# Kernel tuning notes

Measured on AMD Instinct MI355X. Metric: run time of the kernel, lower is better.

Reference implementation:

```python
import jax, jax.numpy as jnp
import numpy as np

# Tree/model constants (perfect binary plan tree in heap layout)
B = 256          # batch of plan trees
DEPTH = 10       # tree depth -> 512 leaves, 511 internal nodes
F = 64           # per-node feature dim
H = 512          # hidden_dim
DV = 64          # data_vec_dim
OUT = 1 + DV     # unit output: latency + data vector
N_LEAF = 2 ** (DEPTH - 1)
N_INT = N_LEAF - 1
N_NODE = N_INT + N_LEAF


def _mlp(x, w0, b0, w1, b1, w2, b2, wo, bo):
    # GenericUnit: num_layers=3 ReLU linears + linear head to OUT
    h = jax.nn.relu(x @ w0 + b0)
    h = jax.nn.relu(h @ w1 + b1)
    h = jax.nn.relu(h @ w2 + b2)
    return h @ wo + bo


def setup_inputs() -> dict:
    key = jax.random.key(0)
    ks = jax.random.split(key, 18)

    def lin(k, fan_in, shape):
        return (jax.random.normal(k, shape, jnp.float32) / np.sqrt(fan_in)).astype(jnp.float32)

    IIN = F + 2 * OUT  # internal unit input: features + two child outputs
    return {
        'leaf_feats': jax.random.normal(ks[0], (B, N_LEAF, F), jnp.float32),
        'internal_feats': jax.random.normal(ks[1], (B, N_INT, F), jnp.float32),
        # leaf unit (0 children)
        'lw0': lin(ks[2], F, (F, H)),   'lb0': jnp.zeros((H,), jnp.float32),
        'lw1': lin(ks[3], H, (H, H)),   'lb1': jnp.zeros((H,), jnp.float32),
        'lw2': lin(ks[4], H, (H, H)),   'lb2': jnp.zeros((H,), jnp.float32),
        'lwo': lin(ks[5], H, (H, OUT)), 'lbo': jnp.zeros((OUT,), jnp.float32),
        # internal unit (2 children)
        'iw0': lin(ks[6], IIN, (IIN, H)), 'ib0': jnp.zeros((H,), jnp.float32),
        'iw1': lin(ks[7], H, (H, H)),     'ib1': jnp.zeros((H,), jnp.float32),
        'iw2': lin(ks[8], H, (H, H)),     'ib2': jnp.zeros((H,), jnp.float32),
        'iwo': lin(ks[9], H, (H, OUT)),   'ibo': jnp.zeros((OUT,), jnp.float32),
    }


def reference(leaf_feats, internal_feats,
              lw0, lb0, lw1, lb1, lw2, lb2, lwo, lbo,
              iw0, ib0, iw1, ib1, iw2, ib2, iwo, ibo):
    # outputs buffer over all nodes, heap layout: internal [0, N_INT), leaves [N_INT, N_NODE)
    out = jnp.zeros((B, N_NODE, OUT), leaf_feats.dtype)
    out = out.at[:, N_INT:].set(_mlp(leaf_feats, lw0, lb0, lw1, lb1, lw2, lb2, lwo, lbo))
    # level-synchronous bottom-up over internal levels (fixed structural loop)
    for l in range(DEPTH - 2, -1, -1):
        s, e = 2 ** l - 1, 2 ** (l + 1) - 1
        left = out[:, 2 * s + 1:2 * e:2]        # children 2i+1
        right = out[:, 2 * s + 2:2 * e + 1:2]   # children 2i+2
        x = jnp.concatenate([internal_feats[:, s:e], left, right], axis=-1)
        out = out.at[:, s:e].set(_mlp(x, iw0, ib0, iw1, ib1, iw2, ib2, iwo, ibo))
    # root latency per tree: output[:, 0] of the root node
    return out[:, 0, 0]
```

## Files before the change

kernel.cpp:

```cpp
#include <hip/hip_runtime.h>
#include <cstdint>
#include <cstddef>
#include <type_traits>

#define OUT_DIM    65
#define TREE_STRIDE 66
#define N_NODE     1023
#define N_INTN     511

typedef _Float16 f16;
typedef _Float16 f16x8 __attribute__((ext_vector_type(8)));
typedef _Float16 f16x4 __attribute__((ext_vector_type(4)));
typedef float    f32x4 __attribute__((ext_vector_type(4)));

template<int V> using ic = std::integral_constant<int, V>;

#define MFMA(a, b, c) __builtin_amdgcn_mfma_f32_16x16x32_f16((a), (b), (c), 0, 0, 0)

template<int VM, int LG>
__device__ __forceinline__ void waitcnt_t() {
  asm volatile("s_waitcnt vmcnt(%0) lgkmcnt(%1)" :: "n"(VM), "n"(LG) : "memory");
}

template<int MT>
__device__ __forceinline__ void storeH_fn(f16* __restrict__ H, f32x4 (&acc)[MT][4],
                                          const float* __restrict__ bias,
                                          int wcb, int quad, int l16) {
#pragma unroll
  for (int mt = 0; mt < MT; mt++) {
#pragma unroll
    for (int nt = 0; nt < 4; nt++) {
      const int c0 = wcb + nt * 16 + quad * 4;
      const float4 bv = *(const float4*)(bias + c0);
      f16x4 hv;
      float v0 = acc[mt][nt][0] + bv.x; hv[0] = (f16)(v0 > 0.f ? v0 : 0.f);
      float v1 = acc[mt][nt][1] + bv.y; hv[1] = (f16)(v1 > 0.f ? v1 : 0.f);
      float v2 = acc[mt][nt][2] + bv.z; hv[2] = (f16)(v2 > 0.f ? v2 : 0.f);
      float v3 = acc[mt][nt][3] + bv.w; hv[3] = (f16)(v3 > 0.f ? v3 : 0.f);
      const int row = mt * 16 + l16;
      *(f16x4*)&H[row * 512 + (((c0 >> 3) ^ l16) << 3) + (quad & 1) * 4] = hv;
    }
  }
}

template<int NC, int MT, int NT, int BD, int AD, bool AGLOB, bool SWAP,
         typename GetB, typename GetA>
__device__ __forceinline__ void kloop(GetB getB, GetA getA, f32x4 (&acc)[MT][NT])
{
  f16x8 bs[BD][NT];
  f16x8 as[AD][MT];
#pragma unroll
  for (int c = 0; c < BD - 1 && c < NC; c++)
#pragma unroll
    for (int nt = 0; nt < NT; nt++) bs[c][nt] = getB(c, nt);
#pragma unroll
  for (int c = 0; c < AD - 1 && c < NC; c++)
#pragma unroll
    for (int mt = 0; mt < MT; mt++) as[c][mt] = getA(c, mt);

  auto lp = [&](auto&& self, auto Cc) -> void {
    constexpr int C = decltype(Cc)::value;
    if constexpr (C < NC) {
      if constexpr (C + BD - 1 < NC) {
#pragma unroll
        for (int nt = 0; nt < NT; nt++) bs[(C + BD - 1) % BD][nt] = getB(C + BD - 1, nt);
      }
      if constexpr (C + AD - 1 < NC) {
#pragma unroll
        for (int mt = 0; mt < MT; mt++) as[(C + AD - 1) % AD][mt] = getA(C + AD - 1, mt);
      }
      constexpr int BOUT = (BD - 1) < (NC - 1 - C) ? (BD - 1) : (NC - 1 - C);
      constexpr int AOUT = (AD - 1) < (NC - 1 - C) ? (AD - 1) : (NC - 1 - C);
      if constexpr (AGLOB) waitcnt_t<0, 0>();
      else                 waitcnt_t<NT * BOUT, MT * AOUT>();
      __builtin_amdgcn_s_setprio(1);
#pragma unroll
      for (int mt = 0; mt < MT; mt++)
#pragma unroll
        for (int nt = 0; nt < NT; nt++)
          acc[mt][nt] = SWAP ? MFMA(bs[C % BD][nt], as[C % AD][mt], acc[mt][nt])
                             : MFMA(as[C % AD][mt], bs[C % BD][nt], acc[mt][nt]);
      __builtin_amdgcn_s_setprio(0);
      self(self, ic<C + 1>{});
    }
  };
  lp(lp, ic<0>{});
}

template<int K, bool AGLOB, typename GetA>
__device__ __forceinline__ void run_layer(
    const f16* __restrict__ Wt, const float* __restrict__ bias,
    f16* __restrict__ H, int wave, int lane, int quad, int l16, GetA getA)
{
  constexpr int NC = K / 32;
  const int wcb = wave * 64;
  const f16* bbase = Wt + (long)(wave * 4) * 512 + lane * 8;
  auto getB = [&](int c, int nt) -> f16x8 {
    return *(const f16x8*)(bbase + (long)(c * 32 + nt) * 512);
  };
  f32x4 acc[4][4];
#pragma unroll
  for (int i = 0; i < 4; i++)
#pragma unroll
    for (int j = 0; j < 4; j++) acc[i][j] = f32x4{0.f, 0.f, 0.f, 0.f};

  kloop<NC, 4, 4, 4, 2, AGLOB, true>(getB, getA, acc);

  __syncthreads();
  storeH_fn<4>(H, acc, bias, wcb, quad, l16);
  __syncthreads();
}

__global__ __launch_bounds__(512, 2) void fused_mlp(
    const float* __restrict__ feats,
    const f16* __restrict__ w0t, const float* __restrict__ b0,
    const f16* __restrict__ w1t, const float* __restrict__ b1,
    const f16* __restrict__ w2t, const float* __restrict__ b2,
    const f16* __restrict__ wot, const float* __restrict__ bo,
    f16* __restrict__ tree, float* __restrict__ dOut, int lvl, int leaf)
{
  extern __shared__ f16 S[];
  f16* H = S;
  f16* X = S;

  const int tid  = threadIdx.x;
  const int wave = tid >> 6;
  const int lane = tid & 63;
  const int quad = lane >> 4;
  const int l16  = lane & 15;
  const long rowBase = (long)blockIdx.x * 64;

  if (!leaf) {
    for (int i = tid; i < 4096; i += 512) {
      int r = i >> 6, cc = i & 63;
      long rg = rowBase + r;
      long bbr = rg >> lvl;
      long ii = rg - (bbr << lvl);
      long nn = (1L << lvl) - 1 + ii;
      X[r * 232 + cc] = (f16)feats[(bbr * N_INTN + nn) * 64 + cc];
    }
    for (int i = tid; i < 4224; i += 512) {
      int r = i / 66, c = i - r * 66;
      long rg = rowBase + r;
      long bbr = rg >> lvl;
      long ii = rg - (bbr << lvl);
      long nn = (1L << lvl) - 1 + ii;
      const uint32_t* src = (const uint32_t*)(tree + (bbr * N_NODE + 2 * nn + 1) * TREE_STRIDE);
      *(uint32_t*)(X + r * 232 + 64 + 2 * c) = src[c];
    }
    for (int i = tid; i < 1792; i += 512) {
      int r = i / 28, cc = i - r * 28;
      X[r * 232 + 196 + cc] = (f16)0.f;
    }
    __syncthreads();
  }

  if (leaf) {
    auto gA = [&](int c, int mt) -> f16x8 {
      const float4* p = (const float4*)(feats + (rowBase + mt * 16 + l16) * 64 + c * 32 + quad * 8);
      float4 u0 = p[0], u1 = p[1];
      f16x8 a;
      a[0] = (f16)u0.x; a[1] = (f16)u0.y; a[2] = (f16)u0.z; a[3] = (f16)u0.w;
      a[4] = (f16)u1.x; a[5] = (f16)u1.y; a[6] = (f16)u1.z; a[7] = (f16)u1.w;
      return a;
    };
    run_layer<64, true>(w0t, b0, H, wave, lane, quad, l16, gA);
  } else {
    auto gA = [&](int c, int mt) -> f16x8 {
      int row = mt * 16 + l16;
      return *(const f16x8*)&X[row * 232 + c * 32 + quad * 8];
    };
    run_layer<224, false>(w0t, b0, H, wave, lane, quad, l16, gA);
  }

  auto getAH = [&](int c, int mt) -> f16x8 {
    int row = mt * 16 + l16;
    return *(const f16x8*)&H[row * 512 + ((((c * 4 + quad) ^ l16) << 3))];
  };
  run_layer<512, false>(w1t, b1, H, wave, lane, quad, l16, getAH);
  run_layer<512, false>(w2t, b2, H, wave, lane, quad, l16, getAH);

  {
    auto doOut = [&](auto NTc, int cb0, int g) {
      constexpr int NT = decltype(NTc)::value;
      const int orow = g * 16 + l16;
      auto gA = [&](int c, int mt) -> f16x8 {
        return *(const f16x8*)&H[orow * 512 + ((((c * 4 + quad) ^ l16) << 3))];
      };
      const long rgb = rowBase + g * 16 + quad * 4;
      const f16* obase = wot + (long)cb0 * 512 + lane * 8;
      auto gB = [&](int c, int nt) -> f16x8 {
        return *(const f16x8*)(obase + (long)(c * 5 + nt) * 512);
      };
      f32x4 oacc[1][NT];
#pragma unroll
      for (int i = 0; i < NT; i++) oacc[0][i] = f32x4{0.f, 0.f, 0.f, 0.f};

      kloop<16, 1, NT, 3, 2, false, false>(gB, gA, oacc);

      f16* tptr[4];
#pragma unroll
      for (int r = 0; r < 4; r++) {
        long rg = rgb + r;
        long b2_ = rg >> lvl;
        long ii  = rg - (b2_ << lvl);
        long node = (1L << lvl) - 1 + ii;
        tptr[r] = tree + (b2_ * N_NODE + node) * TREE_STRIDE;
      }
#pragma unroll
      for (int nt = 0; nt < NT; nt++)
#pragma unroll
        for (int r = 0; r < 4; r++) {
          int col = (cb0 + nt) * 16 + l16;
          if (col < OUT_DIM) {
            float v = oacc[0][nt][r] + bo[col];
            tptr[r][col] = (f16)v;
            if (lvl == 0 && col == 0) dOut[rgb + r] = v;
          } else if (col == OUT_DIM) {
            tptr[r][col] = (f16)0.f;
          }
        }
    };
    if (leaf) {
      if (wave < 4) doOut(ic<5>{}, 0, wave);
    } else {
      const int g = wave & 3, cp = wave >> 2;
      if (cp == 0) doOut(ic<3>{}, 0, g);
      else         doOut(ic<2>{}, 3, g);
    }
  }
}

struct WSeg { const float* W; f16* Wt; int K, N, NB, hole, start; };
struct WPack { WSeg s[8]; int total; };

__global__ void wcast_all(WPack p) {
  int idx = blockIdx.x * 256 + threadIdx.x;
  if (idx >= p.total) return;
  int si = 0;
#pragma unroll
  for (int i = 1; i < 8; i++) if (idx >= p.s[i].start) si = i;
  WSeg sg = p.s[si];
  int e = idx - sg.start;
  int j = e & 7, lane = (e >> 3) & 63, q = e >> 9;
  int cb = q % sg.NB, c = q / sg.NB;
  int col = cb * 16 + (lane & 15);
  int k = c * 32 + (lane >> 4) * 8 + j;
  int srck = (k < sg.hole) ? k : k - 1;
  float v = (k != sg.hole && srck < sg.K && col < sg.N)
                ? sg.W[(long)srck * sg.N + col] : 0.f;
  sg.Wt[e] = (f16)v;
}

extern "C" void kernel_launch(void* const* d_in, const int* in_sizes, int n_in,
                              void* d_out, int out_size, void* d_ws, size_t ws_size,
                              hipStream_t stream) {
  const float* leaf_feats     = (const float*)d_in[0];
  const float* internal_feats = (const float*)d_in[1];
  const float* lw0 = (const float*)d_in[2];
  const float* lb0 = (const float*)d_in[3];
  const float* lw1 = (const float*)d_in[4];
  const float* lb1 = (const float*)d_in[5];
  const float* lw2 = (const float*)d_in[6];
  const float* lb2 = (const float*)d_in[7];
  const float* lwo = (const float*)d_in[8];
  const float* lbo = (const float*)d_in[9];
  const float* iw0 = (const float*)d_in[10];
  const float* ib0 = (const float*)d_in[11];
  const float* iw1 = (const float*)d_in[12];
  const float* ib1 = (const float*)d_in[13];
  const float* iw2 = (const float*)d_in[14];
  const float* ib2 = (const float*)d_in[15];
  const float* iwo = (const float*)d_in[16];
  const float* ibo = (const float*)d_in[17];
  float* dOut = (float*)d_out;

  char* ws = (char*)d_ws;
  size_t off = 0;
  auto alloc = [&](size_t bytes) -> void* {
    void* p = ws + off;
    off += (bytes + 255) & ~(size_t)255;
    return p;
  };

  f16* lw0t = (f16*)alloc((size_t)64  * 512 * 2);
  f16* lw1t = (f16*)alloc((size_t)512 * 512 * 2);
  f16* lw2t = (f16*)alloc((size_t)512 * 512 * 2);
  f16* lwot = (f16*)alloc((size_t)512 * 80  * 2);
  f16* iw0t = (f16*)alloc((size_t)224 * 512 * 2);
  f16* iw1t = (f16*)alloc((size_t)512 * 512 * 2);
  f16* iw2t = (f16*)alloc((size_t)512 * 512 * 2);
  f16* iwot = (f16*)alloc((size_t)512 * 80  * 2);
  f16* tree = (f16*)alloc((size_t)256 * N_NODE * TREE_STRIDE * 2);

  const int NOHOLE = 1 << 30;
  WPack p;
  int cum = 0;
  auto seg = [&](int i, const float* W, f16* Wt, int K, int N, int Kpad, int NB, int hole) {
    p.s[i] = {W, Wt, K, N, NB, hole, cum};
    cum += Kpad * NB * 16;
  };
  seg(0, lw0, lw0t, 64, 512, 64, 32, NOHOLE);
  seg(1, lw1, lw1t, 512, 512, 512, 32, NOHOLE);
  seg(2, lw2, lw2t, 512, 512, 512, 32, NOHOLE);
  seg(3, lwo, lwot, 512, 65, 512, 5, NOHOLE);
  seg(4, iw0, iw0t, 194, 512, 224, 32, 129);
  seg(5, iw1, iw1t, 512, 512, 512, 32, NOHOLE);
  seg(6, iw2, iw2t, 512, 512, 512, 32, NOHOLE);
  seg(7, iwo, iwot, 512, 65, 512, 5, NOHOLE);
  p.total = cum;
  wcast_all<<<dim3((cum + 255) / 256), dim3(256), 0, stream>>>(p);

  static bool attrSet = false;
  if (!attrSet) {
    hipFuncSetAttribute(reinterpret_cast<const void*>(fused_mlp),
                        hipFuncAttributeMaxDynamicSharedMemorySize, 65536);
    attrSet = true;
  }

  const size_t shmem = 65536;

  fused_mlp<<<dim3(2048), dim3(512), shmem, stream>>>(
      leaf_feats, lw0t, lb0, lw1t, lb1, lw2t, lb2, lwot, lbo, tree, dOut, 9, 1);

  for (int l = 8; l >= 0; l--) {
    fused_mlp<<<dim3(4u << l), dim3(512), shmem, stream>>>(
        internal_feats, iw0t, ib0, iw1t, ib1, iw2t, ib2, iwot, ibo, tree, dOut, l, 0);
  }

  (void)in_sizes; (void)n_in; (void)out_size; (void)ws_size;
}
```

Baseline: 631.9 us.

## Fuse the last six tree levels into one persistent tail kernel

```diff
diff --git a/kernel.cpp b/kernel.cpp
--- a/kernel.cpp
+++ b/kernel.cpp
@@ -229,6 +229,119 @@
       else         doOut(ic<2>{}, 3, g);
     }
   }
+}
+
+__global__ __launch_bounds__(512, 2) void tail_mlp(
+    const float* __restrict__ feats,
+    const f16* __restrict__ w0t, const float* __restrict__ b0,
+    const f16* __restrict__ w1t, const float* __restrict__ b1,
+    const f16* __restrict__ w2t, const float* __restrict__ b2,
+    const f16* __restrict__ wot, const float* __restrict__ bo,
+    const f16* __restrict__ tree, float* __restrict__ dOut)
+{
+  extern __shared__ f16 S[];
+  f16* H   = S;
+  f16* X   = S;
+  f16* CB0 = S + 32768;
+  f16* CB1 = S + 36992;
+
+  const long b   = blockIdx.x;
+  const int tid  = threadIdx.x;
+  const int wave = tid >> 6;
+  const int lane = tid & 63;
+  const int quad = lane >> 4;
+  const int l16  = lane & 15;
+
+  auto getAH = [&](int c, int mt) -> f16x8 {
+    int row = mt * 16 + l16;
+    return *(const f16x8*)&H[row * 512 + ((((c * 4 + quad) ^ l16) << 3))];
+  };
+  auto gAX = [&](int c, int mt) -> f16x8 {
+    int row = mt * 16 + l16;
+    return *(const f16x8*)&X[row * 232 + c * 32 + quad * 8];
+  };
+
+  auto level = [&](auto Lc) {
+    constexpr int L = decltype(Lc)::value;
+    constexpr int m = 1 << L;
+    constexpr int R = 2 * m;
+    constexpr int p = (5 - L) & 1;
+    f16* curC  = p ? CB1 : CB0;
+    f16* prevC = p ? CB0 : CB1;
+
+    for (int i = tid; i < 4096; i += 512) {
+      int r = i >> 6, cc = i & 63;
+      int rv = r < R ? r : R - 1;
+      long batch = 2 * b + (rv >> L);
+      long nn = (m - 1) + (rv & (m - 1));
+      X[r * 232 + cc] = (f16)feats[(batch * N_INTN + nn) * 64 + cc];
+    }
+    for (int i = tid; i < 4224; i += 512) {
+      int r = i / 66, c = i - r * 66;
+      int rv = r < R ? r : R - 1;
+      const uint32_t* src;
+      if constexpr (L == 5) {
+        long batch = 2 * b + (rv >> 5);
+        long nn = 31 + (rv & 31);
+        src = (const uint32_t*)(tree + (batch * N_NODE + 2 * nn + 1) * TREE_STRIDE);
+      } else {
+        int cr = ((rv >= m) ? 2 * m : 0) + 2 * (rv & (m - 1));
+        src = (const uint32_t*)(prevC + cr * 66);
+      }
+      *(uint32_t*)(X + r * 232 + 64 + 2 * c) = src[c];
+    }
+    for (int i = tid; i < 1792; i += 512) {
+      int r = i / 28, cc = i - r * 28;
+      X[r * 232 + 196 + cc] = (f16)0.f;
+    }
+    __syncthreads();
+
+    run_layer<224, false>(w0t, b0, H, wave, lane, quad, l16, gAX);
+    run_layer<512, false>(w1t, b1, H, wave, lane, quad, l16, getAH);
+    run_layer<512, false>(w2t, b2, H, wave, lane, quad, l16, getAH);
+
+    if (wave < 4) {
+      const int orow = wave * 16 + l16;
+      auto gA = [&](int c, int mt) -> f16x8 {
+        return *(const f16x8*)&H[orow * 512 + ((((c * 4 + quad) ^ l16) << 3))];
+      };
+      const f16* obase = wot + lane * 8;
+      auto gB = [&](int c, int nt) -> f16x8 {
+        return *(const f16x8*)(obase + (long)(c * 5 + nt) * 512);
+      };
+      f32x4 oacc[1][5];
+#pragma unroll
+      for (int i = 0; i < 5; i++) oacc[0][i] = f32x4{0.f, 0.f, 0.f, 0.f};
+
+      kloop<16, 1, 5, 3, 2, false, false>(gB, gA, oacc);
+
+      const int rowb = wave * 16 + quad * 4;
+#pragma unroll
+      for (int nt = 0; nt < 5; nt++)
+#pragma unroll
+        for (int r = 0; r < 4; r++) {
+          int col = nt * 16 + l16;
+          int row = rowb + r;
+          if (row < R) {
+            if (col < OUT_DIM) {
+              float v = oacc[0][nt][r] + bo[col];
+              if constexpr (L > 0) curC[row * 66 + col] = (f16)v;
+              else { if (col == 0) dOut[2 * b + row] = v; }
+            } else if (col == OUT_DIM) {
+              if constexpr (L > 0) curC[row * 66 + col] = (f16)0.f;
+            }
+          }
+        }
+    }
+    __syncthreads();
+  };
+
+  level(ic<5>{});
+  level(ic<4>{});
+  level(ic<3>{});
+  level(ic<2>{});
+  level(ic<1>{});
+  level(ic<0>{});
 }
 
 struct WSeg { const float* W; f16* Wt; int K, N, NB, hole, start; };
@@ -315,18 +428,24 @@
   if (!attrSet) {
     hipFuncSetAttribute(reinterpret_cast<const void*>(fused_mlp),
                         hipFuncAttributeMaxDynamicSharedMemorySize, 65536);
+    hipFuncSetAttribute(reinterpret_cast<const void*>(tail_mlp),
+                        hipFuncAttributeMaxDynamicSharedMemorySize, 82432);
     attrSet = true;
   }
 
-  const size_t shmem = 65536;
+  const size_t shmem     = 65536;
+  const size_t tailShmem = 82432;
 
   fused_mlp<<<dim3(2048), dim3(512), shmem, stream>>>(
       leaf_feats, lw0t, lb0, lw1t, lb1, lw2t, lb2, lwot, lbo, tree, dOut, 9, 1);
 
-  for (int l = 8; l >= 0; l--) {
+  for (int l = 8; l >= 6; l--) {
     fused_mlp<<<dim3(4u << l), dim3(512), shmem, stream>>>(
         internal_feats, iw0t, ib0, iw1t, ib1, iw2t, ib2, iwot, ibo, tree, dOut, l, 0);
   }
 
+  tail_mlp<<<dim3(128), dim3(512), tailShmem, stream>>>(
+      internal_feats, iw0t, ib0, iw1t, ib1, iw2t, ib2, iwot, ibo, tree, dOut);
+
   (void)in_sizes; (void)n_in; (void)out_size; (void)ws_size;
 }
```

New measurement: 828.4 us. +31.1%, slower.
